# Optimization experiments

Measured on AMD Instinct MI355X. Metric: run time of the kernel, lower is better.

Reference implementation:

```python
import jax, jax.numpy as jnp
import numpy as np

B, C, H, W = 32, 512, 56, 56
GROUPS = 32
CG = C // GROUPS  # channels per group = 16
EPS = 1e-5


def setup_inputs() -> dict:
    key = jax.random.key(0)
    ks = jax.random.split(key, 5)
    return {
        "x": jax.random.normal(ks[0], (B, C, H, W), jnp.float32),
        "w1": jax.random.normal(ks[1], (CG, CG), jnp.float32) * 0.1,   # conv1x1 weight [out,in]
        "b1": jax.random.normal(ks[2], (CG,), jnp.float32) * 0.1,
        "w3": jax.random.normal(ks[3], (CG, CG, 3, 3), jnp.float32) * 0.05,  # conv3x3 OIHW
        "b3": jax.random.normal(ks[4], (CG,), jnp.float32) * 0.1,
        "gn_w": jnp.ones((CG,), jnp.float32),
        "gn_b": jnp.zeros((CG,), jnp.float32),
    }


def reference(x, w1, b1, w3, b3, gn_w, gn_b):
    b, c, h, w = x.shape
    bg = b * GROUPS
    gx = x.reshape(bg, CG, h, w)                                  # group_x
    # directional pooling
    x_h = gx.mean(axis=3, keepdims=True)                          # [bg,cg,h,1]
    x_w = gx.mean(axis=2, keepdims=True).transpose(0, 1, 3, 2)    # [bg,cg,w,1]
    y = jnp.concatenate([x_h, x_w], axis=2)                       # [bg,cg,h+w,1]
    # conv1x1 == channel mixing
    y = jnp.einsum('oc,bcld->bold', w1, y) + b1[None, :, None, None]
    xh = jax.nn.sigmoid(y[:, :, :h])                              # [bg,cg,h,1]
    xw = jax.nn.sigmoid(y[:, :, h:].transpose(0, 1, 3, 2))        # [bg,cg,1,w]
    # GroupNorm(num_groups=cg, num_channels=cg) == per-channel instance norm
    x1 = gx * xh * xw
    mu = x1.mean(axis=(2, 3), keepdims=True)
    var = x1.var(axis=(2, 3), keepdims=True)
    x1 = (x1 - mu) * jax.lax.rsqrt(var + EPS) * gn_w[None, :, None, None] + gn_b[None, :, None, None]
    # conv3x3 branch
    x2 = jax.lax.conv_general_dilated(
        gx, w3, (1, 1), 'SAME',
        dimension_numbers=('NCHW', 'OIHW', 'NCHW')) + b3[None, :, None, None]
    # cross attention weights
    a1 = jax.nn.softmax(x1.mean(axis=(2, 3)), axis=-1)            # [bg,cg]
    a2 = jax.nn.softmax(x2.mean(axis=(2, 3)), axis=-1)            # [bg,cg]
    x1f = x1.reshape(bg, CG, h * w)
    x2f = x2.reshape(bg, CG, h * w)
    out1 = jnp.einsum('bc,bcl->bl', a1, x2f)                      # [bg,hw]
    out2 = jnp.einsum('bc,bcl->bl', a2, x1f)                      # [bg,hw]
    weights = (out1 + out2).reshape(bg, 1, h, w)
    out = gx * jax.nn.sigmoid(weights)
    return out.reshape(b, c, h, w)
```

## Files before the change

### kernel.cpp

```cpp
#include <hip/hip_runtime.h>
#include <math.h>

#define GROUPS 32
#define CG 16
#define HH 56
#define WW 56
#define HW (HH*WW)
#define BG 1024
#define EPS 1e-5f

#define RB 8
#define NB 7
#define LROW 60
#define CSTR (10*LROW)
#define PSTR 452

__global__ __launch_bounds__(256) void kA(const float* __restrict__ x,
        const float* __restrict__ w1, const float* __restrict__ b1,
        const float* __restrict__ w3, const float* __restrict__ b3,
        const float* __restrict__ gn_w, const float* __restrict__ gn_b,
        float* __restrict__ ws_xh, float* __restrict__ ws_xw,
        float* __restrict__ ws_asc, float* __restrict__ ws_aofs,
        float* __restrict__ ws_wa)
{
    const int g = blockIdx.x;
    const int tid = threadIdx.x;
    const float* gx = x + (size_t)g * CG * HW;

    __shared__ float s_row[CG][HH];
    __shared__ float s_col[CG][WW];
    __shared__ float s_xh[CG][HH];
    __shared__ float s_xw[CG][WW];
    __shared__ float ls1[CG], ls2[CG];
    __shared__ float s_x2[CG];

    if (g == 0 && tid < CG * 9 + 1) {
        float m = gn_b[0];
        #pragma unroll
        for (int c = 1; c < CG; ++c) m = fmaxf(m, gn_b[c]);
        float a1[CG]; float den = 0.f;
        #pragma unroll
        for (int c = 0; c < CG; ++c) { a1[c] = __expf(gn_b[c] - m); den += a1[c]; }
        float inv = 1.f / den;
        if (tid < CG * 9) {
            int ci = tid / 9, k = tid - (tid / 9) * 9;
            float s = 0.f;
            #pragma unroll
            for (int o = 0; o < CG; ++o) s += a1[o] * w3[(size_t)(o * CG + ci) * 9 + k];
            ws_wa[tid] = s * inv;
        } else {
            float s = 0.f;
            #pragma unroll
            for (int o = 0; o < CG; ++o) s += a1[o] * b3[o];
            ws_wa[CG * 9] = s * inv;
        }
    }

    {
        const int grp = tid >> 4;
        const int q   = tid & 15;
        const float* pc = gx + grp * HW;
        float c0 = 0.f, c1 = 0.f, c2 = 0.f, c3 = 0.f;
        #pragma unroll 4
        for (int row = 0; row < HH; ++row) {
            float4 v = make_float4(0.f, 0.f, 0.f, 0.f);
            if (q < 14) v = *(const float4*)(pc + row * WW + q * 4);
            c0 += v.x; c1 += v.y; c2 += v.z; c3 += v.w;
            float rs = (v.x + v.y) + (v.z + v.w);
            rs += __shfl_down(rs, 8);
            rs += __shfl_down(rs, 4);
            rs += __shfl_down(rs, 2);
            rs += __shfl_down(rs, 1);
            if (q == 0) s_row[grp][row] = rs * (1.0f / WW);
        }
        if (q < 14) {
            s_col[grp][q * 4 + 0] = c0 * (1.0f / HH);
            s_col[grp][q * 4 + 1] = c1 * (1.0f / HH);
            s_col[grp][q * 4 + 2] = c2 * (1.0f / HH);
            s_col[grp][q * 4 + 3] = c3 * (1.0f / HH);
        }
    }
    __syncthreads();

    for (int t = tid; t < 2 * CG * HH; t += 256) {
        int hpart = (t < CG * HH);
        int tt = hpart ? t : t - CG * HH;
        int o = tt / HH, i = tt - (tt / HH) * HH;
        float v = b1[o];
        #pragma unroll
        for (int c = 0; c < CG; ++c)
            v += w1[o * CG + c] * (hpart ? s_row[c][i] : s_col[c][i]);
        float sg = 1.f / (1.f + __expf(-v));
        if (hpart) { s_xh[o][i] = sg; ws_xh[(size_t)g * CG * HH + tt] = sg; }
        else       { s_xw[o][i] = sg; ws_xw[(size_t)g * CG * WW + tt] = sg; }
    }

    if (tid < CG) {
        ls1[tid] = 0.f; ls2[tid] = 0.f;
        const int o = tid;
        float acc = (float)HW * b3[o];
        for (int c = 0; c < CG; ++c) {
            float S = 0.f;
            #pragma unroll
            for (int r = 0; r < HH; ++r) S += s_row[c][r];
            S *= (float)WW;
            float R0 = (float)WW * s_row[c][HH - 1];
            float R2 = (float)WW * s_row[c][0];
            float C0 = (float)HH * s_col[c][WW - 1];
            float C2 = (float)HH * s_col[c][0];
            const float* p = gx + c * HW;
            float e00 = p[0], e0N = p[WW - 1];
            float eN0 = p[(HH - 1) * WW], eNN = p[(HH - 1) * WW + WW - 1];
            const float* wp = w3 + (size_t)(o * CG + c) * 9;
            #pragma unroll
            for (int dy = 0; dy < 3; ++dy) {
                float Rv = (dy == 0) ? R0 : (dy == 2 ? R2 : 0.f);
                #pragma unroll
                for (int dx = 0; dx < 3; ++dx) {
                    float Cv = (dx == 0) ? C0 : (dx == 2 ? C2 : 0.f);
                    float T = S - Rv - Cv;
                    if (dy != 1 && dx != 1)
                        T += (dy == 0) ? ((dx == 0) ? eNN : eN0)
                                       : ((dx == 0) ? e0N : e00);
                    acc += wp[dy * 3 + dx] * T;
                }
            }
        }
        s_x2[tid] = acc;
    }
    __syncthreads();

    for (int c = 0; c < CG; ++c) {
        float s1 = 0.f, s2 = 0.f;
        const float4* p = (const float4*)(gx + c * HW);
        for (int idx = tid; idx < HW / 4; idx += 256) {
            int l = idx * 4;
            int yy = l / WW, xb = l - yy * WW;
            float4 v = p[idx];
            float xh = s_xh[c][yy];
            float t0 = v.x * xh * s_xw[c][xb];
            float t1 = v.y * xh * s_xw[c][xb + 1];
            float t2 = v.z * xh * s_xw[c][xb + 2];
            float t3 = v.w * xh * s_xw[c][xb + 3];
            s1 += (t0 + t1) + (t2 + t3);
            s2 += (t0 * t0 + t1 * t1) + (t2 * t2 + t3 * t3);
        }
        #pragma unroll
        for (int off = 32; off; off >>= 1) {
            s1 += __shfl_down(s1, off);
            s2 += __shfl_down(s2, off);
        }
        if ((tid & 63) == 0) {
            atomicAdd(&ls1[c], s1);
            atomicAdd(&ls2[c], s2);
        }
    }
    __syncthreads();

    if (tid < CG) {
        float mu  = ls1[tid] * (1.0f / HW);
        float var = ls2[tid] * (1.0f / HW) - mu * mu;
        float sc  = gn_w[tid] * rsqrtf(var + EPS);
        float sh  = gn_b[tid] - mu * sc;

        float v2 = s_x2[tid] * (1.0f / HW);
        float m = v2;
        #pragma unroll
        for (int off = 8; off; off >>= 1) m = fmaxf(m, __shfl_xor(m, off));
        float e = __expf(v2 - m);
        float den = e;
        #pragma unroll
        for (int off = 8; off; off >>= 1) den += __shfl_xor(den, off);
        float a2 = e / den;

        ws_asc[(size_t)g * CG + tid] = a2 * sc;
        float part = a2 * sh;
        #pragma unroll
        for (int off = 8; off; off >>= 1) part += __shfl_xor(part, off);
        if (tid == 0) ws_aofs[g] = part;
    }
}

__global__ __launch_bounds__(256) void kBC(const float* __restrict__ x,
        const float* __restrict__ ws_xh, const float* __restrict__ ws_xw,
        const float* __restrict__ ws_asc, const float* __restrict__ ws_aofs,
        const float* __restrict__ ws_wa, float* __restrict__ out)
{
    const int g = blockIdx.x / NB;
    const int band = blockIdx.x - g * NB;
    const int y0 = band * RB;
    const int tid = threadIdx.x;
    const float* gx = x + (size_t)g * CG * HW;
    float* og = out + (size_t)g * CG * HW;

    __shared__ float s_in[CG * CSTR];
    __shared__ float s_part[4 * PSTR];
    __shared__ float s_xw[CG][WW];
    __shared__ float s_gh[CG][RB];
    __shared__ float s_wa[CG][9];
    __shared__ float s_bias;

    if (tid < CG * (RB + 2)) {
        int c = tid / (RB + 2), r = tid - c * (RB + 2);
        *(float4*)&s_in[c * CSTR + r * LROW] = make_float4(0.f, 0.f, 0.f, 0.f);
    }
    for (int t = tid; t < CG * WW; t += 256)
        s_xw[t / WW][t - (t / WW) * WW] = ws_xw[(size_t)g * CG * WW + t];
    if (tid < CG * RB) {
        int c = tid / RB, r = tid - (tid / RB) * RB;
        s_gh[c][r] = ws_asc[(size_t)g * CG + c]
                   * ws_xh[(size_t)g * CG * HH + c * HH + y0 + r];
    }
    if (tid >= 64 && tid < 64 + CG * 9) {
        int t = tid - 64;
        s_wa[t / 9][t - (t / 9) * 9] = ws_wa[t];
    }
    if (tid == 0) s_bias = ws_wa[CG * 9] + ws_aofs[g];

    for (int t = tid; t < CG * (RB + 2) * (WW / 4); t += 256) {
        int c = t / ((RB + 2) * (WW / 4));
        int rem = t - c * ((RB + 2) * (WW / 4));
        int r = rem / (WW / 4), q = rem - r * (WW / 4);
        int ry = y0 - 1 + r;
        float4 v = make_float4(0.f, 0.f, 0.f, 0.f);
        if (ry >= 0 && ry < HH)
            v = *(const float4*)(gx + c * HW + ry * WW + q * 4);
        *(float4*)&s_in[c * CSTR + r * LROW + 4 + q * 4] = v;
    }
    __syncthreads();

    if (tid < 224) {
        const int cgrp = tid / 56;
        const int s = tid - cgrp * 56;
        const int yl = s / 7;
        const int x0 = (s - yl * 7) * 8;
        const int e1c = (x0 < 48) ? (x0 + 12) : 0;
        float acc[8];
        #pragma unroll
        for (int j = 0; j < 8; ++j) acc[j] = 0.f;

        #pragma unroll
        for (int ci = 0; ci < 4; ++ci) {
            const int c = cgrp * 4 + ci;
            const float* base = &s_in[c * CSTR];
            const float* wp = s_wa[c];
            float w0 = wp[0], w1v = wp[1], w2 = wp[2];
            float w3v = wp[3], w4 = wp[4], w5 = wp[5];
            float w6 = wp[6], w7 = wp[7], w8 = wp[8];
            #pragma unroll
            for (int dy = 0; dy < 3; ++dy) {
                const float* rp = base + (yl + dy) * LROW;
                float e0  = rp[x0 + 3];
                float4 V0 = *(const float4*)(rp + x0 + 4);
                float4 V1 = *(const float4*)(rp + x0 + 8);
                float e1  = rp[e1c];
                float win[10] = {e0, V0.x, V0.y, V0.z, V0.w,
                                 V1.x, V1.y, V1.z, V1.w, e1};
                float a0 = (dy == 0) ? w0 : ((dy == 1) ? w3v : w6);
                float a1 = (dy == 0) ? w1v : ((dy == 1) ? w4 : w7);
                float a2 = (dy == 0) ? w2 : ((dy == 1) ? w5 : w8);
                #pragma unroll
                for (int j = 0; j < 8; ++j)
                    acc[j] += a0 * win[j] + a1 * win[j + 1] + a2 * win[j + 2];
                if (dy == 1) {
                    float gh = s_gh[c][yl];
                    float4 X0 = *(const float4*)(&s_xw[c][x0]);
                    float4 X1 = *(const float4*)(&s_xw[c][x0 + 4]);
                    float xwv[8] = {X0.x, X0.y, X0.z, X0.w,
                                    X1.x, X1.y, X1.z, X1.w};
                    #pragma unroll
                    for (int j = 0; j < 8; ++j)
                        acc[j] += gh * xwv[j] * win[j + 1];
                }
            }
        }
        float* pp = &s_part[cgrp * PSTR + yl * WW + x0];
        *(float4*)pp       = make_float4(acc[0], acc[1], acc[2], acc[3]);
        *(float4*)(pp + 4) = make_float4(acc[4], acc[5], acc[6], acc[7]);
    }
    __syncthreads();

    for (int p = tid; p < RB * WW; p += 256) {
        int yl = p / WW, xx = p - yl * WW;
        float a = s_bias + s_part[p] + s_part[PSTR + p]
                + s_part[2 * PSTR + p] + s_part[3 * PSTR + p];
        float sg = 1.f / (1.f + __expf(-a));
        const float* ctr = &s_in[(yl + 1) * LROW + 4 + xx];
        float* op = og + (y0 + yl) * WW + xx;
        #pragma unroll
        for (int c = 0; c < CG; ++c)
            op[c * HW] = ctr[c * CSTR] * sg;
    }
}

extern "C" void kernel_launch(void* const* d_in, const int* in_sizes, int n_in,
                              void* d_out, int out_size, void* d_ws, size_t ws_size,
                              hipStream_t stream)
{
    const float* x    = (const float*)d_in[0];
    const float* w1   = (const float*)d_in[1];
    const float* b1   = (const float*)d_in[2];
    const float* w3   = (const float*)d_in[3];
    const float* b3   = (const float*)d_in[4];
    const float* gn_w = (const float*)d_in[5];
    const float* gn_b = (const float*)d_in[6];
    float* out = (float*)d_out;

    float* ws = (float*)d_ws;
    float* ws_xh   = ws;
    float* ws_xw   = ws_xh + (size_t)BG * CG * HH;
    float* ws_asc  = ws_xw + (size_t)BG * CG * WW;
    float* ws_aofs = ws_asc + (size_t)BG * CG;
    float* ws_wa   = ws_aofs + (size_t)BG;

    kA<<<BG, 256, 0, stream>>>(x, w1, b1, w3, b3, gn_w, gn_b,
                               ws_xh, ws_xw, ws_asc, ws_aofs, ws_wa);
    kBC<<<BG * NB, 256, 0, stream>>>(x, ws_xh, ws_xw, ws_asc, ws_aofs,
                                     ws_wa, out);
}
```

Before: 498.9 us.

## Parallelize kA stats and conv-mean, halve kBC band height, vectorize output

In kA, the serial per-thread computation of the conv3x3 spatial mean is split. Per-channel statistics go to shared memory first, then all 256 threads each compute one (o,c) partial product. The GroupNorm moment pass becomes a per-channel row-striped loop with shuffle reductions, replacing the shared atomics. In kBC, bands shrink from 8 rows to 4, doubling the block count, each thread covers 2 channels instead of 4, and the final sigmoid/multiply writes float4 vectors. This trades more halo reloads per band for better parallelism and occupancy.

Result: faster. 485.4 us (-2.7%).

```diff
diff --git a/kernel.cpp b/kernel.cpp
--- a/kernel.cpp
+++ b/kernel.cpp
@@ -9,11 +9,12 @@
 #define BG 1024
 #define EPS 1e-5f
 
-#define RB 8
-#define NB 7
+#define RB 4
+#define NB 14
+#define NR (RB+2)
 #define LROW 60
-#define CSTR (10*LROW)
-#define PSTR 452
+#define CSTR (NR*LROW)
+#define PSTR 228
 
 __global__ __launch_bounds__(256) void kA(const float* __restrict__ x,
         const float* __restrict__ w1, const float* __restrict__ b1,
@@ -31,8 +32,9 @@
     __shared__ float s_col[CG][WW];
     __shared__ float s_xh[CG][HH];
     __shared__ float s_xw[CG][WW];
+    __shared__ float s_st[CG][9];
+    __shared__ float s_x2p[CG][CG];
     __shared__ float ls1[CG], ls2[CG];
-    __shared__ float s_x2[CG];
 
     if (g == 0 && tid < CG * 9 + 1) {
         float m = gn_b[0];
@@ -96,74 +98,85 @@
     }
 
     if (tid < CG) {
-        ls1[tid] = 0.f; ls2[tid] = 0.f;
+        const int c = tid;
+        float S = 0.f;
+        #pragma unroll
+        for (int r = 0; r < HH; ++r) S += s_row[c][r];
+        s_st[c][0] = S * (float)WW;
+        s_st[c][1] = (float)WW * s_row[c][HH - 1];
+        s_st[c][2] = (float)WW * s_row[c][0];
+        s_st[c][3] = (float)HH * s_col[c][WW - 1];
+        s_st[c][4] = (float)HH * s_col[c][0];
+        const float* p = gx + c * HW;
+        s_st[c][5] = p[0];
+        s_st[c][6] = p[WW - 1];
+        s_st[c][7] = p[(HH - 1) * WW];
+        s_st[c][8] = p[(HH - 1) * WW + WW - 1];
+    }
+    __syncthreads();
+
+    {
+        const int o = tid >> 4, c = tid & 15;
+        const float* wp = w3 + (size_t)(o * CG + c) * 9;
+        const float* st = s_st[c];
+        float S = st[0];
+        float acc = 0.f;
+        #pragma unroll
+        for (int dy = 0; dy < 3; ++dy) {
+            float Rv = (dy == 0) ? st[1] : (dy == 2 ? st[2] : 0.f);
+            #pragma unroll
+            for (int dx = 0; dx < 3; ++dx) {
+                float Cv = (dx == 0) ? st[3] : (dx == 2 ? st[4] : 0.f);
+                float T = S - Rv - Cv;
+                if (dy != 1 && dx != 1)
+                    T += (dy == 0) ? ((dx == 0) ? st[8] : st[7])
+                                   : ((dx == 0) ? st[6] : st[5]);
+                acc += wp[dy * 3 + dx] * T;
+            }
+        }
+        s_x2p[c][o] = acc;
+    }
+
+    {
+        const int c = tid >> 4;
+        const int q = tid & 15;
+        float s1 = 0.f, s2 = 0.f;
+        if (q < 14) {
+            const float* pc = gx + c * HW;
+            float xw0 = s_xw[c][q * 4 + 0], xw1 = s_xw[c][q * 4 + 1];
+            float xw2 = s_xw[c][q * 4 + 2], xw3v = s_xw[c][q * 4 + 3];
+            #pragma unroll 4
+            for (int row = 0; row < HH; ++row) {
+                float4 v = *(const float4*)(pc + row * WW + q * 4);
+                float xh = s_xh[c][row];
+                float t0 = v.x * xh * xw0;
+                float t1 = v.y * xh * xw1;
+                float t2 = v.z * xh * xw2;
+                float t3 = v.w * xh * xw3v;
+                s1 += (t0 + t1) + (t2 + t3);
+                s2 += (t0 * t0 + t1 * t1) + (t2 * t2 + t3 * t3);
+            }
+        }
+        s1 += __shfl_down(s1, 8);  s2 += __shfl_down(s2, 8);
+        s1 += __shfl_down(s1, 4);  s2 += __shfl_down(s2, 4);
+        s1 += __shfl_down(s1, 2);  s2 += __shfl_down(s2, 2);
+        s1 += __shfl_down(s1, 1);  s2 += __shfl_down(s2, 1);
+        if (q == 0) { ls1[c] = s1; ls2[c] = s2; }
+    }
+    __syncthreads();
+
+    if (tid < CG) {
         const int o = tid;
-        float acc = (float)HW * b3[o];
-        for (int c = 0; c < CG; ++c) {
-            float S = 0.f;
-            #pragma unroll
-            for (int r = 0; r < HH; ++r) S += s_row[c][r];
-            S *= (float)WW;
-            float R0 = (float)WW * s_row[c][HH - 1];
-            float R2 = (float)WW * s_row[c][0];
-            float C0 = (float)HH * s_col[c][WW - 1];
-            float C2 = (float)HH * s_col[c][0];
-            const float* p = gx + c * HW;
-            float e00 = p[0], e0N = p[WW - 1];
-            float eN0 = p[(HH - 1) * WW], eNN = p[(HH - 1) * WW + WW - 1];
-            const float* wp = w3 + (size_t)(o * CG + c) * 9;
-            #pragma unroll
-            for (int dy = 0; dy < 3; ++dy) {
-                float Rv = (dy == 0) ? R0 : (dy == 2 ? R2 : 0.f);
-                #pragma unroll
-                for (int dx = 0; dx < 3; ++dx) {
-                    float Cv = (dx == 0) ? C0 : (dx == 2 ? C2 : 0.f);
-                    float T = S - Rv - Cv;
-                    if (dy != 1 && dx != 1)
-                        T += (dy == 0) ? ((dx == 0) ? eNN : eN0)
-                                       : ((dx == 0) ? e0N : e00);
-                    acc += wp[dy * 3 + dx] * T;
-                }
-            }
-        }
-        s_x2[tid] = acc;
-    }
-    __syncthreads();
-
-    for (int c = 0; c < CG; ++c) {
-        float s1 = 0.f, s2 = 0.f;
-        const float4* p = (const float4*)(gx + c * HW);
-        for (int idx = tid; idx < HW / 4; idx += 256) {
-            int l = idx * 4;
-            int yy = l / WW, xb = l - yy * WW;
-            float4 v = p[idx];
-            float xh = s_xh[c][yy];
-            float t0 = v.x * xh * s_xw[c][xb];
-            float t1 = v.y * xh * s_xw[c][xb + 1];
-            float t2 = v.z * xh * s_xw[c][xb + 2];
-            float t3 = v.w * xh * s_xw[c][xb + 3];
-            s1 += (t0 + t1) + (t2 + t3);
-            s2 += (t0 * t0 + t1 * t1) + (t2 * t2 + t3 * t3);
-        }
-        #pragma unroll
-        for (int off = 32; off; off >>= 1) {
-            s1 += __shfl_down(s1, off);
-            s2 += __shfl_down(s2, off);
-        }
-        if ((tid & 63) == 0) {
-            atomicAdd(&ls1[c], s1);
-            atomicAdd(&ls2[c], s2);
-        }
-    }
-    __syncthreads();
-
-    if (tid < CG) {
-        float mu  = ls1[tid] * (1.0f / HW);
-        float var = ls2[tid] * (1.0f / HW) - mu * mu;
-        float sc  = gn_w[tid] * rsqrtf(var + EPS);
-        float sh  = gn_b[tid] - mu * sc;
-
-        float v2 = s_x2[tid] * (1.0f / HW);
+        float x2 = (float)HW * b3[o];
+        #pragma unroll
+        for (int c = 0; c < CG; ++c) x2 += s_x2p[c][o];
+
+        float mu  = ls1[o] * (1.0f / HW);
+        float var = ls2[o] * (1.0f / HW) - mu * mu;
+        float sc  = gn_w[o] * rsqrtf(var + EPS);
+        float sh  = gn_b[o] - mu * sc;
+
+        float v2 = x2 * (1.0f / HW);
         float m = v2;
         #pragma unroll
         for (int off = 8; off; off >>= 1) m = fmaxf(m, __shfl_xor(m, off));
@@ -173,11 +186,11 @@
         for (int off = 8; off; off >>= 1) den += __shfl_xor(den, off);
         float a2 = e / den;
 
-        ws_asc[(size_t)g * CG + tid] = a2 * sc;
+        ws_asc[(size_t)g * CG + o] = a2 * sc;
         float part = a2 * sh;
         #pragma unroll
         for (int off = 8; off; off >>= 1) part += __shfl_xor(part, off);
-        if (tid == 0) ws_aofs[g] = part;
+        if (o == 0) ws_aofs[g] = part;
     }
 }
 
@@ -194,14 +207,14 @@
     float* og = out + (size_t)g * CG * HW;
 
     __shared__ float s_in[CG * CSTR];
-    __shared__ float s_part[4 * PSTR];
+    __shared__ float s_part[8 * PSTR];
     __shared__ float s_xw[CG][WW];
     __shared__ float s_gh[CG][RB];
     __shared__ float s_wa[CG][9];
     __shared__ float s_bias;
 
-    if (tid < CG * (RB + 2)) {
-        int c = tid / (RB + 2), r = tid - c * (RB + 2);
+    if (tid < CG * NR) {
+        int c = tid / NR, r = tid - c * NR;
         *(float4*)&s_in[c * CSTR + r * LROW] = make_float4(0.f, 0.f, 0.f, 0.f);
     }
     for (int t = tid; t < CG * WW; t += 256)
@@ -211,15 +224,15 @@
         s_gh[c][r] = ws_asc[(size_t)g * CG + c]
                    * ws_xh[(size_t)g * CG * HH + c * HH + y0 + r];
     }
-    if (tid >= 64 && tid < 64 + CG * 9) {
-        int t = tid - 64;
+    if (tid >= 96 && tid < 96 + CG * 9) {
+        int t = tid - 96;
         s_wa[t / 9][t - (t / 9) * 9] = ws_wa[t];
     }
-    if (tid == 0) s_bias = ws_wa[CG * 9] + ws_aofs[g];
-
-    for (int t = tid; t < CG * (RB + 2) * (WW / 4); t += 256) {
-        int c = t / ((RB + 2) * (WW / 4));
-        int rem = t - c * ((RB + 2) * (WW / 4));
+    if (tid == 240) s_bias = ws_wa[CG * 9] + ws_aofs[g];
+
+    for (int t = tid; t < CG * NR * (WW / 4); t += 256) {
+        int c = t / (NR * (WW / 4));
+        int rem = t - c * (NR * (WW / 4));
         int r = rem / (WW / 4), q = rem - r * (WW / 4);
         int ry = y0 - 1 + r;
         float4 v = make_float4(0.f, 0.f, 0.f, 0.f);
@@ -230,8 +243,8 @@
     __syncthreads();
 
     if (tid < 224) {
-        const int cgrp = tid / 56;
-        const int s = tid - cgrp * 56;
+        const int cgrp = tid / 28;
+        const int s = tid - cgrp * 28;
         const int yl = s / 7;
         const int x0 = (s - yl * 7) * 8;
         const int e1c = (x0 < 48) ? (x0 + 12) : 0;
@@ -240,8 +253,8 @@
         for (int j = 0; j < 8; ++j) acc[j] = 0.f;
 
         #pragma unroll
-        for (int ci = 0; ci < 4; ++ci) {
-            const int c = cgrp * 4 + ci;
+        for (int ci = 0; ci < 2; ++ci) {
+            const int c = cgrp * 2 + ci;
             const float* base = &s_in[c * CSTR];
             const float* wp = s_wa[c];
             float w0 = wp[0], w1v = wp[1], w2 = wp[2];
@@ -280,16 +293,35 @@
     }
     __syncthreads();
 
-    for (int p = tid; p < RB * WW; p += 256) {
-        int yl = p / WW, xx = p - yl * WW;
-        float a = s_bias + s_part[p] + s_part[PSTR + p]
-                + s_part[2 * PSTR + p] + s_part[3 * PSTR + p];
-        float sg = 1.f / (1.f + __expf(-a));
-        const float* ctr = &s_in[(yl + 1) * LROW + 4 + xx];
-        float* op = og + (y0 + yl) * WW + xx;
-        #pragma unroll
-        for (int c = 0; c < CG; ++c)
-            op[c * HW] = ctr[c * CSTR] * sg;
+    if (tid < 224) {
+        const int cg2 = tid / 56;
+        const int qd = tid - cg2 * 56;
+        const int yl = qd / 14;
+        const int xq = qd - yl * 14;
+        const int po = yl * WW + xq * 4;
+
+        float4 a = make_float4(s_bias, s_bias, s_bias, s_bias);
+        #pragma unroll
+        for (int cg = 0; cg < 8; ++cg) {
+            float4 pv = *(const float4*)&s_part[cg * PSTR + po];
+            a.x += pv.x; a.y += pv.y; a.z += pv.z; a.w += pv.w;
+        }
+        float4 sg;
+        sg.x = 1.f / (1.f + __expf(-a.x));
+        sg.y = 1.f / (1.f + __expf(-a.y));
+        sg.z = 1.f / (1.f + __expf(-a.z));
+        sg.w = 1.f / (1.f + __expf(-a.w));
+
+        const int coff = (yl + 1) * LROW + 4 + xq * 4;
+        float* ob = og + (y0 + yl) * WW + xq * 4;
+        #pragma unroll
+        for (int ci = 0; ci < 4; ++ci) {
+            const int c = cg2 * 4 + ci;
+            float4 v = *(const float4*)&s_in[c * CSTR + coff];
+            float4 o4 = make_float4(v.x * sg.x, v.y * sg.y,
+                                    v.z * sg.z, v.w * sg.w);
+            *(float4*)(ob + c * HW) = o4;
+        }
     }
 }
 
```
